# Optimization experiments

Measured on AMD Instinct MI355X. Metric: run time of the kernel, lower is better.

## Reference

```python
import jax, jax.numpy as jnp
import numpy as np

PERIOD = 24
NUM_ITERATIONS = 2


def _window_size():
    w = max(3, PERIOD // 2)  # 12
    if w % 2 == 0:
        w += 1  # 13
    return w


def moving_average(s, w):
    # s: [N, L]; replicate-pad by w//2 on each side, then width-w mean conv ('VALID')
    pad = w // 2
    sp = jnp.pad(s, ((0, 0), (pad, pad)), mode='edge')[:, None, :]  # [N,1,L+2*pad]
    k = jnp.ones((1, 1, w), s.dtype) / w
    y = jax.lax.conv_general_dilated(sp, k, window_strides=(1,), padding='VALID',
                                     dimension_numbers=('NCH', 'OIH', 'NCH'))
    return y[:, 0, :]  # [N, L]


def extract_seasonal(d):
    # d: [N, L] with L a multiple of PERIOD. Strided indices i, i+P, ... correspond
    # to reshape [N, C, P] with fixed last axis; median over cycles, broadcast back.
    N, L = d.shape
    C = L // PERIOD
    sub = d.reshape(N, C, PERIOD)
    med = jnp.median(sub, axis=1)  # [N, P] (C=121 is odd -> matches torch.median)
    return jnp.broadcast_to(med[:, None, :], (N, C, PERIOD)).reshape(N, L)


def setup_inputs() -> dict:
    key = jax.random.key(0)
    x = jax.random.normal(key, (64, 2904, 207), dtype=jnp.float32)
    return {"x": x}


def reference(x):
    # x: [B, L, F] -> process all features at once as [B*F, L]
    B, L, F = x.shape
    s = jnp.transpose(x, (0, 2, 1)).reshape(B * F, L)
    w = _window_size()
    trend = moving_average(s, w)
    for _ in range(NUM_ITERATIONS):
        seasonal = extract_seasonal(s - trend)
        trend = moving_average(s - seasonal, w)
    residual = s - trend - seasonal

    def unflatten(a):
        return jnp.transpose(a.reshape(B, F, L), (0, 2, 1))  # [B, L, F]

    return unflatten(trend), unflatten(seasonal), unflatten(residual)
```

## Files before the change

kernel.cpp:

```cpp
#include <hip/hip_runtime.h>

#define LROW    2904
#define PERIOD  24
#define CYC     121
#define NT      256
#define NF      207
#define NB      64
#define NROWS   13248
#define CHUNK   (NROWS / 8)
#define LTILE   24
#define NLT     (LROW / LTILE)
#define K2GRID  (NB * NLT)
#define K2CHUNK (K2GRID / 8)
#define CSTR    133

__device__ __forceinline__ int clampi(int i) {
    return i < 0 ? 0 : (i >= LROW ? LROW - 1 : i);
}

__device__ __forceinline__ unsigned quantk(float d) {
    int ki = (int)fmaf(d, 4096.f, 32768.f);
    ki = ki < 0 ? 0 : (ki > 65535 ? 65535 : ki);
    return (unsigned)ki;
}
__device__ __forceinline__ float reconk(unsigned pref) {
    return ((float)(int)pref - 32767.5f) * (1.f / 4096.f);
}

__device__ __forceinline__ float ws_edge(int l, const float* lmed) {
    float w = 0.f;
    #pragma unroll
    for (int j = -6; j <= 6; ++j) {
        int idx = clampi(l + j);
        int ph = (idx < PERIOD) ? idx : idx - 2880;
        w += lmed[ph];
    }
    return w;
}

__device__ __forceinline__ void sel60x2(unsigned a0, unsigned a1,
                                        unsigned b0, unsigned b1,
                                        unsigned& prefA, unsigned& prefB) {
    int actA = __shfl(121, 0);
    int actB = actA;
    int rA = 60, rB = 60;
    unsigned pA = 0, pB = 0;
    #pragma unroll
    for (int bit = 15; bit >= 0; --bit) {
        unsigned wA = (pA << 1) | 1u;
        unsigned wB = (pB << 1) | 1u;
        unsigned long long mA0 = __ballot((a0 >> bit) == wA);
        unsigned long long mA1 = __ballot((a1 >> bit) == wA);
        unsigned long long mB0 = __ballot((b0 >> bit) == wB);
        unsigned long long mB1 = __ballot((b1 >> bit) == wB);
        int onesA = __popcll(mA0) + __popcll(mA1);
        int onesB = __popcll(mB0) + __popcll(mB1);
        int zA = actA - onesA, zB = actB - onesB;
        bool tA = (rA >= zA), tB = (rB >= zB);
        pA = tA ? wA : wA - 1u;  pB = tB ? wB : wB - 1u;
        rA = tA ? rA - zA : rA;  rB = tB ? rB - zB : rB;
        actA = tA ? onesA : zA;  actB = tB ? onesB : zB;
    }
    prefA = pA; prefB = pB;
}

__global__ __launch_bounds__(NT, 6) void stl_medians(const float* __restrict__ x,
                                                     float* __restrict__ ws) {
    __shared__ float At[PERIOD][CSTR];
    __shared__ float SAt[PERIOD][CSTR];
    __shared__ float lmedA[PERIOD];
    __shared__ float lmedB[PERIOD];
    __shared__ float Wtab[PERIOD];

    const int d   = blockIdx.x;
    const int row = (d & 7) * CHUNK + (d >> 3);
    const int b = row / NF;
    const int f = row - b * NF;
    const int t = threadIdx.x;
    const size_t rowbase = (size_t)b * (LROW * NF) + (size_t)f;

    {
        int l = t, c = t / PERIOD, p = t - c * PERIOD;
        while (l < LROW) {
            At[p][c] = x[rowbase + (size_t)l * NF];
            l += NT; p += 16; c += 10;
            if (p >= PERIOD) { p -= PERIOD; ++c; }
        }
    }
    __syncthreads();

    if (t < 242) {
        const int h  = (t >= 121) ? 1 : 0;
        const int c  = t - 121 * h;
        const int pb = 12 * h;
        const int l0 = c * PERIOD + pb;
        float s = 0.f;
        #pragma unroll
        for (int j = -6; j <= 6; ++j) {
            int lm = clampi(l0 + j);
            s += At[lm % PERIOD][lm / PERIOD];
        }
        SAt[pb][c] = s;
        #pragma unroll
        for (int q = 1; q < 12; ++q) {
            int la = clampi(l0 + q + 6), lr = clampi(l0 + q - 7);
            s += At[la % PERIOD][la / PERIOD] - At[lr % PERIOD][lr / PERIOD];
            SAt[pb + q][c] = s;
        }
    }
    __syncthreads();

    const int wid  = t >> 6;
    const int lane = t & 63;
    const int c1   = 64 + lane;
    const bool has1 = (c1 < CYC);

    #pragma unroll
    for (int pr = 0; pr < 3; ++pr) {
        const int pA = wid * 6 + pr * 2, pB = pA + 1;
        unsigned a0 = quantk(At[pA][lane] - SAt[pA][lane] * (1.f / 13.f));
        unsigned b0 = quantk(At[pB][lane] - SAt[pB][lane] * (1.f / 13.f));
        unsigned a1 = 0xFFFFFFFFu, b1 = 0xFFFFFFFFu;
        if (has1) {
            a1 = quantk(At[pA][c1] - SAt[pA][c1] * (1.f / 13.f));
            b1 = quantk(At[pB][c1] - SAt[pB][c1] * (1.f / 13.f));
        }
        unsigned prA, prB;
        sel60x2(a0, a1, b0, b1, prA, prB);
        if (lane == 0) { lmedA[pA] = reconk(prA); lmedA[pB] = reconk(prB); }
    }
    __syncthreads();
    if (t < PERIOD) {
        float w = 0.f;
        #pragma unroll
        for (int j = 0; j < 13; ++j) {
            int ph = t + j; if (ph >= PERIOD) ph -= PERIOD;
            w += lmedA[ph];
        }
        Wtab[t] = w;
    }
    __syncthreads();

    #pragma unroll 1
    for (int rep = 0; rep < 2; ++rep) {
        const int j = (rep == 0) ? wid : (wid < 2 ? 4 + wid : 99);
        if (j > 5) continue;
        const int pA = j, pB = 18 + j;
        const float wA = Wtab[j + 18];
        const float wB = Wtab[j + 12];
        float wA0 = (lane == 0) ? ws_edge(pA, lmedA) : wA;
        unsigned a0 = quantk(At[pA][lane] - (SAt[pA][lane] - wA0) * (1.f / 13.f));
        unsigned b0 = quantk(At[pB][lane] - (SAt[pB][lane] - wB)  * (1.f / 13.f));
        unsigned a1 = 0xFFFFFFFFu, b1 = 0xFFFFFFFFu;
        if (has1) {
            float wB1 = (lane == 56) ? ws_edge(2880 + pB, lmedA) : wB;
            a1 = quantk(At[pA][c1] - (SAt[pA][c1] - wA)  * (1.f / 13.f));
            b1 = quantk(At[pB][c1] - (SAt[pB][c1] - wB1) * (1.f / 13.f));
        }
        unsigned prA, prB;
        sel60x2(a0, a1, b0, b1, prA, prB);
        if (lane == 0) { lmedB[pA] = reconk(prA); lmedB[pB] = reconk(prB); }
    }
    __syncthreads();
    if (t < PERIOD) {
        if (t >= 6 && t < 18)
            lmedB[t] = lmedA[t] + Wtab[t - 6] * (1.f / 13.f);
        float w = 0.f;
        #pragma unroll
        for (int j2 = 0; j2 < 13; ++j2) {
            int ph = t + j2; if (ph >= PERIOD) ph -= PERIOD;
            w += lmedB[ph];
        }
        Wtab[t] = w;
    }
    __syncthreads();

    if (t < 48) {
        int isW = (t >= 24);
        int p2  = t - (isW ? 24 : 0);
        ws[((size_t)b * 48 + t) * NF + f] = isW ? Wtab[p2] : lmedB[p2];
    }
}

__global__ __launch_bounds__(NT, 5) void stl_outputs(const float* __restrict__ x,
                                                     const float* __restrict__ ws,
                                                     float* __restrict__ out) {
    __shared__ float T[(LTILE + 12) * NF];

    const int d   = blockIdx.x;
    const int blk = (d & 7) * K2CHUNK + (d >> 3);
    const int b  = blk / NLT;
    const int kk = blk - b * NLT;
    const int l0 = kk * LTILE;
    const int t  = threadIdx.x;
    const float* xb = x + (size_t)b * (LROW * NF);

    if (kk != 0 && kk != NLT - 1) {
        const float2* s2 = (const float2*)(xb + (size_t)(l0 - 6) * NF);
        float2* t2 = (float2*)T;
        for (int i = t; i < (LTILE + 12) * NF / 2; i += NT) t2[i] = s2[i];
    } else {
        for (int i = t; i < (LTILE + 12) * NF; i += NT) {
            int lr = i / NF;
            int ff = i - lr * NF;
            T[i] = xb[(size_t)clampi(l0 - 6 + lr) * NF + ff];
        }
    }
    __syncthreads();

    if (t < NF) {
        float lm[PERIOD], wt[PERIOD];
        const float* wrow = ws + (size_t)b * 48 * NF + t;
        #pragma unroll
        for (int i = 0; i < PERIOD; ++i) lm[i] = wrow[i * NF];
        #pragma unroll
        for (int i = 0; i < PERIOD; ++i) wt[i] = wrow[(PERIOD + i) * NF];

        float s13 = 0.f;
        #pragma unroll
        for (int r = 0; r < 13; ++r) s13 += T[r * NF + t];

        const bool edgeLo = (kk == 0), edgeHi = (kk == NLT - 1);
        const size_t S = (size_t)NROWS * LROW;
        const size_t obase = (size_t)b * (LROW * NF) + (size_t)l0 * NF + (size_t)t;

        #pragma unroll
        for (int j = 0; j < LTILE; ++j) {
            float W = wt[(j + 18) % 24];
            if (edgeLo && j < 6) {
                float w = 0.f;
                #pragma unroll
                for (int jj = -6; jj <= 6; ++jj) { int m = j + jj; if (m < 0) m = 0; w += lm[m]; }
                W = w;
            }
            if (edgeHi && j >= 18) {
                float w = 0.f;
                #pragma unroll
                for (int jj = -6; jj <= 6; ++jj) { int m = j + jj; if (m > 23) m = 23; w += lm[m]; }
                W = w;
            }
            float tr = (s13 - W) * (1.f / 13.f);
            float se = lm[j];
            float re = T[(j + 6) * NF + t] - tr - se;
            size_t o = obase + (size_t)(j * NF);
            __builtin_nontemporal_store(tr, &out[o]);
            __builtin_nontemporal_store(se, &out[S + o]);
            __builtin_nontemporal_store(re, &out[2 * S + o]);
            if (j < LTILE - 1)
                s13 += T[(j + 13) * NF + t] - T[j * NF + t];
        }
    }
}

extern "C" void kernel_launch(void* const* d_in, const int* in_sizes, int n_in,
                              void* d_out, int out_size, void* d_ws, size_t ws_size,
                              hipStream_t stream) {
    const float* x = (const float*)d_in[0];
    float* out = (float*)d_out;
    float* ws  = (float*)d_ws;
    (void)in_sizes; (void)n_in; (void)out_size; (void)ws_size;
    hipLaunchKernelGGL(stl_medians, dim3(NROWS), dim3(NT), 0, stream, x, ws);
    hipLaunchKernelGGL(stl_outputs, dim3(K2GRID), dim3(NT), 0, stream, x, ws, out);
}
```

Measured before the change: 378.7 us.

## Pre-transpose input via tiled kernel so median kernel reads rows contiguously

Adds a shared-memory tiled transpose kernel that writes x as [B*F, L] into workspace, and a templated median kernel that loads each row with contiguous float4 reads instead of strided per-element gathers with stride NF. This is meant to remove uncoalesced global reads in the first pass. In exchange it adds an extra full read and write of the input (~154MB of traffic) plus a kernel launch, and it falls back to the old path when the workspace is too small.

```diff
diff --git a/kernel.cpp b/kernel.cpp
--- a/kernel.cpp
+++ b/kernel.cpp
@@ -13,6 +13,8 @@
 #define K2GRID  (NB * NLT)
 #define K2CHUNK (K2GRID / 8)
 #define CSTR    133
+#define TD      64
+#define WSTAB   (48 * NB * NF)
 
 __device__ __forceinline__ int clampi(int i) {
     return i < 0 ? 0 : (i >= LROW ? LROW - 1 : i);
@@ -64,7 +66,27 @@
     prefA = pA; prefB = pB;
 }
 
-__global__ __launch_bounds__(NT, 6) void stl_medians(const float* __restrict__ x,
+__global__ __launch_bounds__(256) void transpose_k(const float* __restrict__ x,
+                                                   float* __restrict__ xT) {
+    __shared__ float tile[TD][TD + 1];
+    const int f0 = blockIdx.x * TD;
+    const int l0 = blockIdx.y * TD;
+    const int b  = blockIdx.z;
+    const int t  = threadIdx.x;
+    const int tx = t & 63, ty = t >> 6;
+    const int lmax = min(TD, LROW - l0);
+    const int fmax = min(TD, NF - f0);
+    const float* xb = x + (size_t)b * (LROW * NF);
+    for (int i = ty; i < lmax; i += 4)
+        if (tx < fmax) tile[i][tx] = xb[(size_t)(l0 + i) * NF + f0 + tx];
+    __syncthreads();
+    float* xTb = xT + (size_t)b * NF * LROW;
+    for (int i = ty; i < fmax; i += 4)
+        if (tx < lmax) xTb[(size_t)(f0 + i) * LROW + l0 + tx] = tile[tx][i];
+}
+
+template <bool TR>
+__global__ __launch_bounds__(NT, 6) void stl_medians(const float* __restrict__ xin,
                                                      float* __restrict__ ws) {
     __shared__ float At[PERIOD][CSTR];
     __shared__ float SAt[PERIOD][CSTR];
@@ -77,12 +99,24 @@
     const int b = row / NF;
     const int f = row - b * NF;
     const int t = threadIdx.x;
-    const size_t rowbase = (size_t)b * (LROW * NF) + (size_t)f;
-
-    {
+
+    if (TR) {
+        const float4* src4 = (const float4*)(xin + (size_t)row * LROW);
+        for (int i = t; i < LROW / 4; i += NT) {
+            float4 v = src4[i];
+            int l = i * 4;
+            int c = l / PERIOD;
+            int p = l - c * PERIOD;
+            At[p][c]     = v.x;
+            At[p + 1][c] = v.y;
+            At[p + 2][c] = v.z;
+            At[p + 3][c] = v.w;
+        }
+    } else {
+        const size_t rowbase = (size_t)b * (LROW * NF) + (size_t)f;
         int l = t, c = t / PERIOD, p = t - c * PERIOD;
         while (l < LROW) {
-            At[p][c] = x[rowbase + (size_t)l * NF];
+            At[p][c] = xin[rowbase + (size_t)l * NF];
             l += NT; p += 16; c += 10;
             if (p >= PERIOD) { p -= PERIOD; ++c; }
         }
@@ -257,8 +291,18 @@
                               hipStream_t stream) {
     const float* x = (const float*)d_in[0];
     float* out = (float*)d_out;
-    float* ws  = (float*)d_ws;
-    (void)in_sizes; (void)n_in; (void)out_size; (void)ws_size;
-    hipLaunchKernelGGL(stl_medians, dim3(NROWS), dim3(NT), 0, stream, x, ws);
-    hipLaunchKernelGGL(stl_outputs, dim3(K2GRID), dim3(NT), 0, stream, x, ws, out);
-}
+    float* wsTab = (float*)d_ws;
+    float* xT = wsTab + WSTAB;
+    (void)in_sizes; (void)n_in; (void)out_size;
+
+    const size_t need = (size_t)(WSTAB + (size_t)NROWS * LROW) * sizeof(float);
+    if (ws_size >= need) {
+        hipLaunchKernelGGL(transpose_k, dim3(4, 46, NB), dim3(256), 0, stream, x, xT);
+        hipLaunchKernelGGL((stl_medians<true>), dim3(NROWS), dim3(NT), 0, stream,
+                           xT, wsTab);
+    } else {
+        hipLaunchKernelGGL((stl_medians<false>), dim3(NROWS), dim3(NT), 0, stream,
+                           x, wsTab);
+    }
+    hipLaunchKernelGGL(stl_outputs, dim3(K2GRID), dim3(NT), 0, stream, x, wsTab, out);
+}
```

New measurement: 448.0 us. +18.3%, slower.
